# Kernel optimization log

Measured on AMD Instinct MI355X. Metric: run time of the kernel, lower is better.

The kernel has to match this reference:

```python
import jax, jax.numpy as jnp
import numpy as np

N_ENT = 50000
N_REL = 200
DIM = 128
N_BASES = 4
NUM_RELATIONS = 2 * N_REL  # RGCNConv num_relations
E = 200000
S = 20000


def rgcn_conv(x, edge_index, edge_type, edge_norm, basis, att, root, bias, n_nodes):
    """RGCNConv with basis decomposition, aggr='mean'.
    x: [N, Din]; basis: [B, Din, Dout]; att: [R, B]; root: [Din, Dout]; bias: [Dout].
    """
    src, dst = edge_index[0], edge_index[1]
    x_j = x[src]                      # [E, Din] gather
    att_e = att[edge_type]            # [E, B]
    # message: x_j @ (att_e @ basis) without materializing per-edge [Din,Dout] weights
    msg = jnp.einsum('ei,bio,eb->eo', x_j, basis, att_e)  # [E, Dout]
    msg = msg * edge_norm[:, None]
    agg = jax.ops.segment_sum(msg, dst, num_segments=n_nodes)            # [N, Dout]
    cnt = jax.ops.segment_sum(jnp.ones_like(edge_norm), dst, num_segments=n_nodes)
    agg = agg / jnp.maximum(cnt, 1.0)[:, None]            # mean aggregation
    return agg + x @ root + bias


def setup_inputs() -> dict:
    key = jax.random.key(0)
    ks = jax.random.split(key, 20)
    d = {}
    d['entity'] = jnp.arange(N_ENT, dtype=jnp.int64) if jax.config.read('jax_enable_x64') else jnp.arange(N_ENT, dtype=jnp.int32)
    d['edge_index'] = jax.random.randint(ks[0], (2, E), 0, N_ENT)
    d['edge_type'] = jax.random.randint(ks[1], (E,), 0, NUM_RELATIONS)
    d['edge_norm'] = jax.random.uniform(ks[2], (E,), dtype=jnp.float32)
    d['samples'] = jax.random.randint(ks[3], (S, 3), 0, N_REL)
    d['DAD_rel'] = jax.random.normal(ks[4], (N_REL, N_REL), dtype=jnp.float32) * 0.05
    # learned parameters
    d['entity_emb'] = jax.random.normal(ks[5], (N_ENT, DIM), dtype=jnp.float32) * 0.02
    d['relation_emb'] = jax.random.normal(ks[6], (N_REL, DIM), dtype=jnp.float32) * 0.02
    d['entity_context_tab'] = jax.random.normal(ks[7], (N_ENT, DIM), dtype=jnp.float32) * 0.02
    d['relation_context_tab'] = jax.random.normal(ks[8], (N_REL, DIM), dtype=jnp.float32) * 0.02
    d['relation_gcn_weight'] = jax.random.normal(ks[9], (DIM, DIM), dtype=jnp.float32) * 0.02
    d['gate_entity'] = jax.random.uniform(ks[10], (DIM,), dtype=jnp.float32)
    d['gate_relation'] = jax.random.uniform(ks[11], (DIM,), dtype=jnp.float32)
    d['basis1'] = jax.random.normal(ks[12], (N_BASES, DIM, DIM), dtype=jnp.float32) * 0.02
    d['att1'] = jax.random.normal(ks[13], (NUM_RELATIONS, N_BASES), dtype=jnp.float32) * 0.1
    d['root1'] = jax.random.normal(ks[14], (DIM, DIM), dtype=jnp.float32) * 0.02
    d['bias1'] = jnp.zeros((DIM,), dtype=jnp.float32)
    d['basis2'] = jax.random.normal(ks[15], (N_BASES, DIM, DIM), dtype=jnp.float32) * 0.02
    d['att2'] = jax.random.normal(ks[16], (NUM_RELATIONS, N_BASES), dtype=jnp.float32) * 0.1
    d['root2'] = jax.random.normal(ks[17], (DIM, DIM), dtype=jnp.float32) * 0.02
    d['bias2'] = jnp.zeros((DIM,), dtype=jnp.float32)
    return d


def reference(entity, edge_index, edge_type, edge_norm, samples, DAD_rel,
              entity_emb, relation_emb, entity_context_tab, relation_context_tab,
              relation_gcn_weight, gate_entity, gate_relation,
              basis1, att1, root1, bias1, basis2, att2, root2, bias2):
    n_nodes = entity.shape[0]
    ent_ctx = entity_context_tab[entity]                  # [N, D]
    rel_ctx = relation_context_tab                        # arange over all relations -> full table
    ent_ctx = jax.nn.relu(rgcn_conv(ent_ctx, edge_index, edge_type, edge_norm,
                                    basis1, att1, root1, bias1, n_nodes))
    ent_ctx = jax.nn.relu(rgcn_conv(ent_ctx, edge_index, edge_type, edge_norm,
                                    basis2, att2, root2, bias2, n_nodes))
    rel_ctx = jax.nn.relu((DAD_rel @ rel_ctx) @ relation_gcn_weight)
    ge = jax.nn.sigmoid(gate_entity)
    gr = jax.nn.sigmoid(gate_relation)
    h, r, t = samples[:, 0], samples[:, 1], samples[:, 2]
    head_o = ge * entity_emb[h] + (1.0 - ge) * ent_ctx[h]
    rel_o = gr * relation_emb[r] + (1.0 - gr) * rel_ctx[r]
    tail_o = ge * entity_emb[t] + (1.0 - ge) * ent_ctx[t]
    return jnp.stack([head_o, rel_o, tail_o])             # [3, S, D]
```

## Files before the change

kernel.cpp:

```cpp
#include <hip/hip_runtime.h>
#include <hip/hip_bf16.h>

typedef short s8v  __attribute__((ext_vector_type(8)));
typedef float f16v __attribute__((ext_vector_type(16)));

__device__ __forceinline__ unsigned short f2bf(float x) {
    unsigned u = __float_as_uint(x);
    unsigned r = ((u >> 16) & 1u) + 0x7FFFu;
    return (unsigned short)((u + r) >> 16);
}
__device__ __forceinline__ float bf2f(unsigned short h) {
    return __uint_as_float(((unsigned)h) << 16);
}

__global__ __launch_bounds__(256) void x0_kernel(
    const float* __restrict__ tab, const int* __restrict__ entity,
    float* __restrict__ X0, int N)
{
    int idx = blockIdx.x * 256 + threadIdx.x;
    int n = idx >> 5, l = idx & 31;
    if (n < N) {
        int src = entity[n];
        *(float4*)&X0[(size_t)n * 128 + l * 4] =
            *(const float4*)&tab[(size_t)src * 128 + l * 4];
    }
}

__global__ __launch_bounds__(256) void bprep_kernel(
    const float* __restrict__ basis1, const float* __restrict__ root1,
    const float* __restrict__ basis2, const float* __restrict__ root2,
    unsigned short* __restrict__ Bp1h, unsigned short* __restrict__ Bp1l,
    unsigned short* __restrict__ Bp2h, unsigned short* __restrict__ Bp2l)
{
    int idx = blockIdx.x * 256 + threadIdx.x;
    int layer = blockIdx.y;
    int n = idx & 127, k = idx >> 7;
    const float* basis = layer ? basis2 : basis1;
    const float* root  = layer ? root2  : root1;
    float v = (k < 512) ? basis[((k & 3) << 14) + ((k >> 2) << 7) + n]
                        : root[((k - 512) << 7) + n];
    unsigned short h = f2bf(v);
    unsigned short l = f2bf(v - bf2f(h));
    size_t pos = (((size_t)(k >> 3) * 128) + n) * 8 + (k & 7);
    unsigned short* Bh = layer ? Bp2h : Bp1h;
    unsigned short* Bl = layer ? Bp2l : Bp1l;
    Bh[pos] = h;
    Bl[pos] = l;
}

__global__ __launch_bounds__(256) void hist_kernel(
    const int* __restrict__ edge_index, int* __restrict__ deg, int E)
{
    int e = blockIdx.x * 256 + threadIdx.x;
    if (e < E) atomicAdd(&deg[edge_index[E + e]], 1);
}

__global__ __launch_bounds__(1024) void scanA_kernel(
    const int* __restrict__ deg, int* __restrict__ row_start,
    int* __restrict__ btot, int N)
{
    __shared__ int wtot[16];
    __shared__ int woff[16];
    const int tid = threadIdx.x, lane = tid & 63, wid = tid >> 6;
    int i = blockIdx.x * 1024 + tid;
    int v = (i < N) ? deg[i] : 0;
    int x = v;
    #pragma unroll
    for (int d = 1; d < 64; d <<= 1) {
        int t = __shfl_up(x, d, 64);
        if (lane >= d) x += t;
    }
    if (lane == 63) wtot[wid] = x;
    __syncthreads();
    if (wid == 0 && lane < 16) {
        int s = wtot[lane];
        int y = s;
        #pragma unroll
        for (int d = 1; d < 16; d <<= 1) {
            int t = __shfl_up(y, d, 16);
            if (lane >= d) y += t;
        }
        woff[lane] = y - s;
        if (lane == 15) btot[blockIdx.x] = y;
    }
    __syncthreads();
    if (i < N) row_start[i] = woff[wid] + (x - v);
}

__global__ __launch_bounds__(64) void scanB_kernel(
    const int* __restrict__ btot, int* __restrict__ boff,
    int* __restrict__ row_start, int nB, int N)
{
    int t = threadIdx.x;
    int v = (t < nB) ? btot[t] : 0;
    int x = v;
    #pragma unroll
    for (int d = 1; d < 64; d <<= 1) {
        int u = __shfl_up(x, d, 64);
        if (t >= d) x += u;
    }
    if (t < nB) boff[t] = x - v;
    if (t == nB - 1) row_start[N] = x;
}

__global__ __launch_bounds__(1024) void scanC_kernel(
    int* __restrict__ row_start, int* __restrict__ cursor,
    const int* __restrict__ boff, int N)
{
    int i = blockIdx.x * 1024 + threadIdx.x;
    if (i < N) {
        int r = row_start[i] + boff[blockIdx.x];
        row_start[i] = r;
        cursor[i]    = r;
    }
}

__global__ __launch_bounds__(256) void fill_kernel(
    const int* __restrict__ edge_index, const int* __restrict__ edge_type,
    const float* __restrict__ edge_norm, int* __restrict__ cursor,
    const float* __restrict__ att1, const float* __restrict__ att2,
    int* __restrict__ src_s, float4* __restrict__ an1, float4* __restrict__ an2, int E)
{
    int e = blockIdx.x * 256 + threadIdx.x;
    if (e >= E) return;
    int dst = edge_index[E + e];
    int et  = edge_type[e];
    float n = edge_norm[e];
    int pos = atomicAdd(&cursor[dst], 1);
    src_s[pos] = edge_index[e];
    float4 a1 = *(const float4*)&att1[(size_t)et * 4];
    float4 a2 = *(const float4*)&att2[(size_t)et * 4];
    an1[pos] = make_float4(n * a1.x, n * a1.y, n * a1.z, n * a1.w);
    an2[pos] = make_float4(n * a2.x, n * a2.y, n * a2.z, n * a2.w);
}

__global__ __launch_bounds__(256) void edge_agg_kernel(
    const float* __restrict__ X,
    const int* __restrict__ row_start,
    const int* __restrict__ src_s,
    const float4* __restrict__ an,
    unsigned short* __restrict__ w, int N)
{
    int n = blockIdx.x * 8 + (threadIdx.x >> 5);
    if (n >= N) return;
    int l = threadIdx.x & 31;
    int s0 = row_start[n], s1 = row_start[n + 1];
    float acc[4][4];
    #pragma unroll
    for (int d = 0; d < 4; ++d)
        #pragma unroll
        for (int b = 0; b < 4; ++b) acc[d][b] = 0.f;

    for (int p = s0; p < s1; p += 4) {
        int i1 = min(p + 1, s1 - 1);
        int i2 = min(p + 2, s1 - 1);
        int i3 = min(p + 3, s1 - 1);
        int sA = src_s[p],  sB = src_s[i1];
        int sC = src_s[i2], sD = src_s[i3];
        float4 aA = an[p],  aB = an[i1];
        float4 aC = an[i2], aD = an[i3];
        if (p + 1 >= s1) aB = make_float4(0.f, 0.f, 0.f, 0.f);
        if (p + 2 >= s1) aC = make_float4(0.f, 0.f, 0.f, 0.f);
        if (p + 3 >= s1) aD = make_float4(0.f, 0.f, 0.f, 0.f);
        float4 xA = *(const float4*)&X[(size_t)sA * 128 + (l << 2)];
        float4 xB = *(const float4*)&X[(size_t)sB * 128 + (l << 2)];
        float4 xC = *(const float4*)&X[(size_t)sC * 128 + (l << 2)];
        float4 xD = *(const float4*)&X[(size_t)sD * 128 + (l << 2)];
        float xsA[4] = {xA.x, xA.y, xA.z, xA.w};
        float xsB[4] = {xB.x, xB.y, xB.z, xB.w};
        float xsC[4] = {xC.x, xC.y, xC.z, xC.w};
        float xsD[4] = {xD.x, xD.y, xD.z, xD.w};
        #pragma unroll
        for (int d = 0; d < 4; ++d) {
            acc[d][0] = fmaf(aA.x, xsA[d], fmaf(aB.x, xsB[d], fmaf(aC.x, xsC[d], fmaf(aD.x, xsD[d], acc[d][0]))));
            acc[d][1] = fmaf(aA.y, xsA[d], fmaf(aB.y, xsB[d], fmaf(aC.y, xsC[d], fmaf(aD.y, xsD[d], acc[d][1]))));
            acc[d][2] = fmaf(aA.z, xsA[d], fmaf(aB.z, xsB[d], fmaf(aC.z, xsC[d], fmaf(aD.z, xsD[d], acc[d][2]))));
            acc[d][3] = fmaf(aA.w, xsA[d], fmaf(aB.w, xsB[d], fmaf(aC.w, xsC[d], fmaf(aD.w, xsD[d], acc[d][3]))));
        }
    }
    float inv = 1.0f / fmaxf((float)(s1 - s0), 1.0f);
    #pragma unroll
    for (int d = 0; d < 4; ++d) {
        ushort4 h;
        h.x = f2bf(acc[d][0] * inv);
        h.y = f2bf(acc[d][1] * inv);
        h.z = f2bf(acc[d][2] * inv);
        h.w = f2bf(acc[d][3] * inv);
        *(ushort4*)&w[(size_t)n * 512 + (l << 4) + (d << 2)] = h;
    }
}

__global__ __launch_bounds__(256) void gemm640_kernel(
    const unsigned short* __restrict__ wbf,
    const float* __restrict__ X,
    const unsigned short* __restrict__ Bph,
    const unsigned short* __restrict__ Bpl,
    const float* __restrict__ bias,
    float* __restrict__ Xout, int N)
{
    __shared__ unsigned short A_hi[64 * 40];
    __shared__ unsigned short A_lo[64 * 40];

    const int tid  = threadIdx.x;
    const int row0 = blockIdx.x * 64;
    const int lane = tid & 63, wv = tid >> 6;
    const int m    = lane & 31;
    const int kh8  = lane >> 5;
    const int rt   = (wv & 1) << 5;
    const int c0w  = (wv >> 1) << 6;

    const int ar  = tid >> 2;
    const int akv = (tid & 3) << 3;

    const s8v z8 = {0,0,0,0,0,0,0,0};
    s8v pA = z8;
    float4 pX0, pX1;
    s8v B0[8], B1[8];

    auto loadB = [&](int kc, s8v (&dst)[8]) {
        #pragma unroll
        for (int h = 0; h < 2; ++h) {
            int khg = kc * 4 + h * 2 + kh8;
            #pragma unroll
            for (int ct = 0; ct < 2; ++ct) {
                size_t off = ((size_t)khg * 128 + (c0w + ct * 32 + m)) * 8;
                dst[h * 4 + ct * 2 + 0] = *(const s8v*)&Bph[off];
                dst[h * 4 + ct * 2 + 1] = *(const s8v*)&Bpl[off];
            }
        }
    };
    auto loadA = [&](int kc) {
        int k0 = kc * 32;
        int gr = row0 + ar;
        if (k0 < 512) {
            pA = (gr < N) ? *(const s8v*)&wbf[(size_t)gr * 512 + k0 + akv] : z8;
        } else {
            pX0 = make_float4(0.f, 0.f, 0.f, 0.f);
            pX1 = pX0;
            if (gr < N) {
                pX0 = *(const float4*)&X[(size_t)gr * 128 + (k0 - 512) + akv];
                pX1 = *(const float4*)&X[(size_t)gr * 128 + (k0 - 512) + akv + 4];
            }
        }
    };

    f16v acc0, acc1;
    #pragma unroll
    for (int i = 0; i < 16; ++i) { acc0[i] = 0.f; acc1[i] = 0.f; }

    loadA(0);
    loadB(0, B0);

    auto chunk = [&](int kc, s8v (&cur)[8], s8v (&nxt)[8]) {
        const int k0 = kc * 32;
        if (kc) __syncthreads();
        if (k0 < 512) {
            *(s8v*)&A_hi[ar * 40 + akv] = pA;
        } else {
            float f[8] = {pX0.x, pX0.y, pX0.z, pX0.w, pX1.x, pX1.y, pX1.z, pX1.w};
            s8v h8, l8;
            #pragma unroll
            for (int j = 0; j < 8; ++j) {
                unsigned short h = f2bf(f[j]);
                h8[j] = (short)h;
                l8[j] = (short)f2bf(f[j] - bf2f(h));
            }
            *(s8v*)&A_hi[ar * 40 + akv] = h8;
            *(s8v*)&A_lo[ar * 40 + akv] = l8;
        }
        __syncthreads();
        if (kc < 19) { loadA(kc + 1); loadB(kc + 1, nxt); }

        #pragma unroll
        for (int h = 0; h < 2; ++h) {
            const int off = h * 16 + kh8 * 8;
            s8v aH = *(const s8v*)&A_hi[(rt + m) * 40 + off];
            if (k0 < 512) {
                acc0 = __builtin_amdgcn_mfma_f32_32x32x16_bf16(aH, cur[h*4+1], acc0, 0, 0, 0);
                acc0 = __builtin_amdgcn_mfma_f32_32x32x16_bf16(aH, cur[h*4+0], acc0, 0, 0, 0);
                acc1 = __builtin_amdgcn_mfma_f32_32x32x16_bf16(aH, cur[h*4+3], acc1, 0, 0, 0);
                acc1 = __builtin_amdgcn_mfma_f32_32x32x16_bf16(aH, cur[h*4+2], acc1, 0, 0, 0);
            } else {
                s8v aL = *(const s8v*)&A_lo[(rt + m) * 40 + off];
                acc0 = __builtin_amdgcn_mfma_f32_32x32x16_bf16(aL, cur[h*4+0], acc0, 0, 0, 0);
                acc0 = __builtin_amdgcn_mfma_f32_32x32x16_bf16(aH, cur[h*4+1], acc0, 0, 0, 0);
                acc0 = __builtin_amdgcn_mfma_f32_32x32x16_bf16(aH, cur[h*4+0], acc0, 0, 0, 0);
                acc1 = __builtin_amdgcn_mfma_f32_32x32x16_bf16(aL, cur[h*4+2], acc1, 0, 0, 0);
                acc1 = __builtin_amdgcn_mfma_f32_32x32x16_bf16(aH, cur[h*4+3], acc1, 0, 0, 0);
                acc1 = __builtin_amdgcn_mfma_f32_32x32x16_bf16(aH, cur[h*4+2], acc1, 0, 0, 0);
            }
        }
    };

    #pragma unroll 1
    for (int kc2 = 0; kc2 < 10; ++kc2) {
        chunk(kc2 * 2,     B0, B1);
        chunk(kc2 * 2 + 1, B1, B0);
    }

    const int rbase = rt + (kh8 << 2);
    #pragma unroll
    for (int ct = 0; ct < 2; ++ct) {
        int gc = c0w + ct * 32 + m;
        float bv = bias[gc];
        #pragma unroll
        for (int reg = 0; reg < 16; ++reg) {
            int gr = row0 + rbase + (reg & 3) + ((reg >> 2) << 3);
            if (gr < N) {
                float v = ct ? acc1[reg] : acc0[reg];
                Xout[(size_t)gr * 128 + gc] = fmaxf(v + bv, 0.f);
            }
        }
    }
}

__global__ __launch_bounds__(512) void relctx_kernel(
    const float* __restrict__ DAD,
    const float* __restrict__ tab,
    const float* __restrict__ W,
    float* __restrict__ R2, int NR)
{
    __shared__ float part[4][128];
    __shared__ float r1s[128];
    int r = blockIdx.x;
    int t = threadIdx.x;
    int o = t & 127, q = t >> 7;
    float s = 0.f;
    #pragma unroll 4
    for (int j = q; j < NR; j += 4)
        s = fmaf(DAD[r * NR + j], tab[j * 128 + o], s);
    part[q][o] = s;
    __syncthreads();
    if (t < 128) r1s[t] = part[0][t] + part[1][t] + part[2][t] + part[3][t];
    __syncthreads();
    float s2 = 0.f;
    #pragma unroll 8
    for (int k = q * 32; k < q * 32 + 32; ++k)
        s2 = fmaf(r1s[k], W[k * 128 + o], s2);
    part[q][o] = s2;
    __syncthreads();
    if (t < 128)
        R2[r * 128 + t] = fmaxf(part[0][t] + part[1][t] + part[2][t] + part[3][t], 0.f);
}

__global__ __launch_bounds__(256) void output_kernel(
    const int* __restrict__ samples,
    const float* __restrict__ gate_e,
    const float* __restrict__ gate_r,
    const float* __restrict__ ent_emb,
    const float* __restrict__ rel_emb,
    const float* __restrict__ ctx2,
    const float* __restrict__ relctx,
    float* __restrict__ out, int S)
{
    int s = blockIdx.x * 2 + (threadIdx.x >> 7);
    if (s >= S) return;
    int p = blockIdx.y;
    int o = threadIdx.x & 127;
    float v;
    if (p == 1) {
        int idx = samples[s * 3 + 1];
        float g = 1.0f / (1.0f + __expf(-gate_r[o]));
        v = g * rel_emb[idx * 128 + o] + (1.0f - g) * relctx[idx * 128 + o];
    } else {
        int idx = samples[s * 3 + (p == 0 ? 0 : 2)];
        float g = 1.0f / (1.0f + __expf(-gate_e[o]));
        v = g * ent_emb[(size_t)idx * 128 + o] + (1.0f - g) * ctx2[(size_t)idx * 128 + o];
    }
    out[(size_t)p * S * 128 + (size_t)s * 128 + o] = v;
}

extern "C" void kernel_launch(void* const* d_in, const int* in_sizes, int n_in,
                              void* d_out, int out_size, void* d_ws, size_t ws_size,
                              hipStream_t stream)
{
    const int*   entity     = (const int*)d_in[0];
    const int*   edge_index = (const int*)d_in[1];
    const int*   edge_type  = (const int*)d_in[2];
    const float* edge_norm  = (const float*)d_in[3];
    const int*   samples    = (const int*)d_in[4];
    const float* DAD        = (const float*)d_in[5];
    const float* ent_emb    = (const float*)d_in[6];
    const float* rel_emb    = (const float*)d_in[7];
    const float* ent_tab    = (const float*)d_in[8];
    const float* rel_tab    = (const float*)d_in[9];
    const float* Wrel       = (const float*)d_in[10];
    const float* gate_e     = (const float*)d_in[11];
    const float* gate_r     = (const float*)d_in[12];
    const float* basis1     = (const float*)d_in[13];
    const float* att1       = (const float*)d_in[14];
    const float* root1      = (const float*)d_in[15];
    const float* bias1      = (const float*)d_in[16];
    const float* basis2     = (const float*)d_in[17];
    const float* att2       = (const float*)d_in[18];
    const float* root2      = (const float*)d_in[19];
    const float* bias2      = (const float*)d_in[20];

    const int N  = in_sizes[0];
    const int E  = in_sizes[2];
    const int S  = in_sizes[4] / 3;
    const int NR = in_sizes[9] / 128;

    float* ws      = (float*)d_ws;
    float* X0      = ws;
    float* X1      = X0 + (size_t)N * 128;
    float4* an1    = (float4*)(X1 + (size_t)N * 128);
    float4* an2    = an1 + (E + 4);
    unsigned short* wbf = (unsigned short*)(an2 + (E + 4));
    float* Rc      = (float*)(wbf + (size_t)N * 512);
    int*   deg     = (int*)(Rc + (size_t)NR * 128);
    int*   rstart  = deg + N;
    int*   cursor  = rstart + N + 1;
    int*   src_s   = cursor + N;
    int*   btot    = src_s + E + 4;
    int*   boff    = btot + 64;
    uintptr_t bt   = ((uintptr_t)(boff + 64) + 15) & ~(uintptr_t)15;
    unsigned short* Bp1h = (unsigned short*)bt;
    unsigned short* Bp1l = Bp1h + 80 * 128 * 8;
    unsigned short* Bp2h = Bp1l + 80 * 128 * 8;
    unsigned short* Bp2l = Bp2h + 80 * 128 * 8;

    const int egrid = (E + 255) / 256;
    const int ggrid = (N + 63) / 64;
    const int agrid = (N + 7) / 8;
    const int nB    = (N + 1023) / 1024;

    bprep_kernel<<<dim3(320, 2), 256, 0, stream>>>(basis1, root1, basis2, root2,
                                                   Bp1h, Bp1l, Bp2h, Bp2l);
    hipMemsetAsync(deg, 0, (size_t)N * sizeof(int), stream);
    hist_kernel<<<egrid, 256, 0, stream>>>(edge_index, deg, E);
    scanA_kernel<<<nB, 1024, 0, stream>>>(deg, rstart, btot, N);
    scanB_kernel<<<1, 64, 0, stream>>>(btot, boff, rstart, nB, N);
    scanC_kernel<<<nB, 1024, 0, stream>>>(rstart, cursor, boff, N);
    fill_kernel<<<egrid, 256, 0, stream>>>(edge_index, edge_type, edge_norm, cursor,
                                           att1, att2, src_s, an1, an2, E);

    x0_kernel<<<(N * 32 + 255) / 256, 256, 0, stream>>>(ent_tab, entity, X0, N);

    edge_agg_kernel<<<agrid, 256, 0, stream>>>(X0, rstart, src_s, an1, wbf, N);
    gemm640_kernel<<<ggrid, 256, 0, stream>>>(wbf, X0, Bp1h, Bp1l, bias1, X1, N);

    edge_agg_kernel<<<agrid, 256, 0, stream>>>(X1, rstart, src_s, an2, wbf, N);
    gemm640_kernel<<<ggrid, 256, 0, stream>>>(wbf, X1, Bp2h, Bp2l, bias2, X0, N);

    relctx_kernel<<<NR, 512, 0, stream>>>(DAD, rel_tab, Wrel, Rc, NR);

    output_kernel<<<dim3((S + 1) / 2, 3), 256, 0, stream>>>(
        samples, gate_e, gate_r, ent_emb, rel_emb, X0, Rc, (float*)d_out, S);
}
```

Measured before the change: 348.2 us.

## Fuse edge aggregation and basis GEMM into one per-layer kernel via LDS

Merges the edge gather/aggregation kernel and the 640-wide MFMA GEMM into a single layer kernel. Each block aggregates 32 nodes into a swizzled LDS tile holding the bf16 basis coefficients plus the hi/lo split of the root input, then runs the MFMA GEMM directly from LDS. This removes the global round-trip of the N x 512 bf16 intermediate and one launch per layer. In exchange, the GEMM tile shrinks from 64 to 32 rows with 32 columns per wave, so the B matrix is reloaded for every 32 rows. The block also needs about 48KB of LDS, which may lower occupancy during the latency-bound gather phase.

```diff
diff --git a/kernel.cpp b/kernel.cpp
--- a/kernel.cpp
+++ b/kernel.cpp
@@ -134,183 +134,158 @@
     an2[pos] = make_float4(n * a2.x, n * a2.y, n * a2.z, n * a2.w);
 }
 
-__global__ __launch_bounds__(256) void edge_agg_kernel(
+__global__ __launch_bounds__(256) void layer_kernel(
     const float* __restrict__ X,
     const int* __restrict__ row_start,
     const int* __restrict__ src_s,
     const float4* __restrict__ an,
-    unsigned short* __restrict__ w, int N)
-{
-    int n = blockIdx.x * 8 + (threadIdx.x >> 5);
-    if (n >= N) return;
-    int l = threadIdx.x & 31;
-    int s0 = row_start[n], s1 = row_start[n + 1];
-    float acc[4][4];
-    #pragma unroll
-    for (int d = 0; d < 4; ++d)
-        #pragma unroll
-        for (int b = 0; b < 4; ++b) acc[d][b] = 0.f;
-
-    for (int p = s0; p < s1; p += 4) {
-        int i1 = min(p + 1, s1 - 1);
-        int i2 = min(p + 2, s1 - 1);
-        int i3 = min(p + 3, s1 - 1);
-        int sA = src_s[p],  sB = src_s[i1];
-        int sC = src_s[i2], sD = src_s[i3];
-        float4 aA = an[p],  aB = an[i1];
-        float4 aC = an[i2], aD = an[i3];
-        if (p + 1 >= s1) aB = make_float4(0.f, 0.f, 0.f, 0.f);
-        if (p + 2 >= s1) aC = make_float4(0.f, 0.f, 0.f, 0.f);
-        if (p + 3 >= s1) aD = make_float4(0.f, 0.f, 0.f, 0.f);
-        float4 xA = *(const float4*)&X[(size_t)sA * 128 + (l << 2)];
-        float4 xB = *(const float4*)&X[(size_t)sB * 128 + (l << 2)];
-        float4 xC = *(const float4*)&X[(size_t)sC * 128 + (l << 2)];
-        float4 xD = *(const float4*)&X[(size_t)sD * 128 + (l << 2)];
-        float xsA[4] = {xA.x, xA.y, xA.z, xA.w};
-        float xsB[4] = {xB.x, xB.y, xB.z, xB.w};
-        float xsC[4] = {xC.x, xC.y, xC.z, xC.w};
-        float xsD[4] = {xD.x, xD.y, xD.z, xD.w};
-        #pragma unroll
-        for (int d = 0; d < 4; ++d) {
-            acc[d][0] = fmaf(aA.x, xsA[d], fmaf(aB.x, xsB[d], fmaf(aC.x, xsC[d], fmaf(aD.x, xsD[d], acc[d][0]))));
-            acc[d][1] = fmaf(aA.y, xsA[d], fmaf(aB.y, xsB[d], fmaf(aC.y, xsC[d], fmaf(aD.y, xsD[d], acc[d][1]))));
-            acc[d][2] = fmaf(aA.z, xsA[d], fmaf(aB.z, xsB[d], fmaf(aC.z, xsC[d], fmaf(aD.z, xsD[d], acc[d][2]))));
-            acc[d][3] = fmaf(aA.w, xsA[d], fmaf(aB.w, xsB[d], fmaf(aC.w, xsC[d], fmaf(aD.w, xsD[d], acc[d][3]))));
-        }
-    }
-    float inv = 1.0f / fmaxf((float)(s1 - s0), 1.0f);
-    #pragma unroll
-    for (int d = 0; d < 4; ++d) {
-        ushort4 h;
-        h.x = f2bf(acc[d][0] * inv);
-        h.y = f2bf(acc[d][1] * inv);
-        h.z = f2bf(acc[d][2] * inv);
-        h.w = f2bf(acc[d][3] * inv);
-        *(ushort4*)&w[(size_t)n * 512 + (l << 4) + (d << 2)] = h;
-    }
-}
-
-__global__ __launch_bounds__(256) void gemm640_kernel(
-    const unsigned short* __restrict__ wbf,
-    const float* __restrict__ X,
     const unsigned short* __restrict__ Bph,
     const unsigned short* __restrict__ Bpl,
     const float* __restrict__ bias,
     float* __restrict__ Xout, int N)
 {
-    __shared__ unsigned short A_hi[64 * 40];
-    __shared__ unsigned short A_lo[64 * 40];
-
-    const int tid  = threadIdx.x;
-    const int row0 = blockIdx.x * 64;
+    __shared__ unsigned short Whi[80 * 32 * 8];
+    __shared__ unsigned short Wlo[16 * 32 * 8];
+
+    const int tid   = threadIdx.x;
+    const int node0 = blockIdx.x * 32;
+
+    {
+        int g = tid >> 5, l = tid & 31;
+        #pragma unroll 1
+        for (int i = 0; i < 4; ++i) {
+            int n  = g * 4 + i;
+            int gn = node0 + n;
+            float acc[4][4];
+            #pragma unroll
+            for (int d = 0; d < 4; ++d)
+                #pragma unroll
+                for (int b = 0; b < 4; ++b) acc[d][b] = 0.f;
+            float inv = 1.f;
+            if (gn < N) {
+                int s0 = row_start[gn], s1 = row_start[gn + 1];
+                for (int p = s0; p < s1; p += 4) {
+                    int i1 = min(p + 1, s1 - 1);
+                    int i2 = min(p + 2, s1 - 1);
+                    int i3 = min(p + 3, s1 - 1);
+                    int sA = src_s[p],  sB = src_s[i1];
+                    int sC = src_s[i2], sD = src_s[i3];
+                    float4 aA = an[p],  aB = an[i1];
+                    float4 aC = an[i2], aD = an[i3];
+                    if (p + 1 >= s1) aB = make_float4(0.f, 0.f, 0.f, 0.f);
+                    if (p + 2 >= s1) aC = make_float4(0.f, 0.f, 0.f, 0.f);
+                    if (p + 3 >= s1) aD = make_float4(0.f, 0.f, 0.f, 0.f);
+                    float4 xA = *(const float4*)&X[(size_t)sA * 128 + (l << 2)];
+                    float4 xB = *(const float4*)&X[(size_t)sB * 128 + (l << 2)];
+                    float4 xC = *(const float4*)&X[(size_t)sC * 128 + (l << 2)];
+                    float4 xD = *(const float4*)&X[(size_t)sD * 128 + (l << 2)];
+                    float xsA[4] = {xA.x, xA.y, xA.z, xA.w};
+                    float xsB[4] = {xB.x, xB.y, xB.z, xB.w};
+                    float xsC[4] = {xC.x, xC.y, xC.z, xC.w};
+                    float xsD[4] = {xD.x, xD.y, xD.z, xD.w};
+                    #pragma unroll
+                    for (int d = 0; d < 4; ++d) {
+                        acc[d][0] = fmaf(aA.x, xsA[d], fmaf(aB.x, xsB[d], fmaf(aC.x, xsC[d], fmaf(aD.x, xsD[d], acc[d][0]))));
+                        acc[d][1] = fmaf(aA.y, xsA[d], fmaf(aB.y, xsB[d], fmaf(aC.y, xsC[d], fmaf(aD.y, xsD[d], acc[d][1]))));
+                        acc[d][2] = fmaf(aA.z, xsA[d], fmaf(aB.z, xsB[d], fmaf(aC.z, xsC[d], fmaf(aD.z, xsD[d], acc[d][2]))));
+                        acc[d][3] = fmaf(aA.w, xsA[d], fmaf(aB.w, xsB[d], fmaf(aC.w, xsC[d], fmaf(aD.w, xsD[d], acc[d][3]))));
+                    }
+                }
+                inv = 1.0f / fmaxf((float)(s1 - s0), 1.0f);
+            }
+            #pragma unroll
+            for (int d = 0; d < 4; ++d) {
+                int kh   = 2 * l + (d >> 1);
+                int slot = n ^ (kh & 31);
+                ushort4 h;
+                h.x = f2bf(acc[d][0] * inv);
+                h.y = f2bf(acc[d][1] * inv);
+                h.z = f2bf(acc[d][2] * inv);
+                h.w = f2bf(acc[d][3] * inv);
+                *(ushort4*)&Whi[(kh * 32 + slot) * 8 + (d & 1) * 4] = h;
+            }
+        }
+    }
+
+    {
+        int r  = tid >> 3;
+        int kq = (tid & 7) * 16;
+        int gn = node0 + r;
+        float4 v0 = make_float4(0,0,0,0), v1 = v0, v2 = v0, v3 = v0;
+        if (gn < N) {
+            const float* xp = &X[(size_t)gn * 128 + kq];
+            v0 = *(const float4*)(xp + 0);
+            v1 = *(const float4*)(xp + 4);
+            v2 = *(const float4*)(xp + 8);
+            v3 = *(const float4*)(xp + 12);
+        }
+        float f[16] = {v0.x, v0.y, v0.z, v0.w, v1.x, v1.y, v1.z, v1.w,
+                       v2.x, v2.y, v2.z, v2.w, v3.x, v3.y, v3.z, v3.w};
+        #pragma unroll
+        for (int i = 0; i < 2; ++i) {
+            int kh   = 64 + (tid & 7) * 2 + i;
+            int slot = r ^ (kh & 31);
+            s8v h8, l8;
+            #pragma unroll
+            for (int j = 0; j < 8; ++j) {
+                unsigned short h = f2bf(f[i * 8 + j]);
+                h8[j] = (short)h;
+                l8[j] = (short)f2bf(f[i * 8 + j] - bf2f(h));
+            }
+            *(s8v*)&Whi[(kh * 32 + slot) * 8] = h8;
+            *(s8v*)&Wlo[((kh - 64) * 32 + slot) * 8] = l8;
+        }
+    }
+    __syncthreads();
+
     const int lane = tid & 63, wv = tid >> 6;
     const int m    = lane & 31;
     const int kh8  = lane >> 5;
-    const int rt   = (wv & 1) << 5;
-    const int c0w  = (wv >> 1) << 6;
-
-    const int ar  = tid >> 2;
-    const int akv = (tid & 3) << 3;
-
-    const s8v z8 = {0,0,0,0,0,0,0,0};
-    s8v pA = z8;
-    float4 pX0, pX1;
-    s8v B0[8], B1[8];
-
-    auto loadB = [&](int kc, s8v (&dst)[8]) {
+    const int c0   = wv << 5;
+
+    f16v acc;
+    #pragma unroll
+    for (int i = 0; i < 16; ++i) acc[i] = 0.f;
+
+    s8v Bb[2][8];
+    auto loadB4 = [&](int g, int buf) {
         #pragma unroll
-        for (int h = 0; h < 2; ++h) {
-            int khg = kc * 4 + h * 2 + kh8;
-            #pragma unroll
-            for (int ct = 0; ct < 2; ++ct) {
-                size_t off = ((size_t)khg * 128 + (c0w + ct * 32 + m)) * 8;
-                dst[h * 4 + ct * 2 + 0] = *(const s8v*)&Bph[off];
-                dst[h * 4 + ct * 2 + 1] = *(const s8v*)&Bpl[off];
+        for (int q = 0; q < 4; ++q) {
+            int khg = (g * 4 + q) * 2 + kh8;
+            size_t off = ((size_t)khg * 128 + c0 + m) * 8;
+            Bb[buf][q * 2 + 0] = *(const s8v*)&Bph[off];
+            Bb[buf][q * 2 + 1] = *(const s8v*)&Bpl[off];
+        }
+    };
+    loadB4(0, 0);
+
+    #pragma unroll
+    for (int g = 0; g < 10; ++g) {
+        int buf = g & 1;
+        if (g < 9) loadB4(g + 1, buf ^ 1);
+        #pragma unroll
+        for (int q = 0; q < 4; ++q) {
+            int s    = g * 4 + q;
+            int khg  = s * 2 + kh8;
+            int slot = m ^ (khg & 31);
+            s8v aH = *(const s8v*)&Whi[(khg * 32 + slot) * 8];
+            if (s >= 32) {
+                s8v aL = *(const s8v*)&Wlo[((khg - 64) * 32 + slot) * 8];
+                acc = __builtin_amdgcn_mfma_f32_32x32x16_bf16(aL, Bb[buf][q*2], acc, 0, 0, 0);
             }
-        }
-    };
-    auto loadA = [&](int kc) {
-        int k0 = kc * 32;
-        int gr = row0 + ar;
-        if (k0 < 512) {
-            pA = (gr < N) ? *(const s8v*)&wbf[(size_t)gr * 512 + k0 + akv] : z8;
-        } else {
-            pX0 = make_float4(0.f, 0.f, 0.f, 0.f);
-            pX1 = pX0;
-            if (gr < N) {
-                pX0 = *(const float4*)&X[(size_t)gr * 128 + (k0 - 512) + akv];
-                pX1 = *(const float4*)&X[(size_t)gr * 128 + (k0 - 512) + akv + 4];
-            }
-        }
-    };
-
-    f16v acc0, acc1;
+            acc = __builtin_amdgcn_mfma_f32_32x32x16_bf16(aH, Bb[buf][q*2+1], acc, 0, 0, 0);
+            acc = __builtin_amdgcn_mfma_f32_32x32x16_bf16(aH, Bb[buf][q*2+0], acc, 0, 0, 0);
+        }
+    }
+
+    int gc = c0 + m;
+    float bv = bias[gc];
+    const int rbase = kh8 << 2;
     #pragma unroll
-    for (int i = 0; i < 16; ++i) { acc0[i] = 0.f; acc1[i] = 0.f; }
-
-    loadA(0);
-    loadB(0, B0);
-
-    auto chunk = [&](int kc, s8v (&cur)[8], s8v (&nxt)[8]) {
-        const int k0 = kc * 32;
-        if (kc) __syncthreads();
-        if (k0 < 512) {
-            *(s8v*)&A_hi[ar * 40 + akv] = pA;
-        } else {
-            float f[8] = {pX0.x, pX0.y, pX0.z, pX0.w, pX1.x, pX1.y, pX1.z, pX1.w};
-            s8v h8, l8;
-            #pragma unroll
-            for (int j = 0; j < 8; ++j) {
-                unsigned short h = f2bf(f[j]);
-                h8[j] = (short)h;
-                l8[j] = (short)f2bf(f[j] - bf2f(h));
-            }
-            *(s8v*)&A_hi[ar * 40 + akv] = h8;
-            *(s8v*)&A_lo[ar * 40 + akv] = l8;
-        }
-        __syncthreads();
-        if (kc < 19) { loadA(kc + 1); loadB(kc + 1, nxt); }
-
-        #pragma unroll
-        for (int h = 0; h < 2; ++h) {
-            const int off = h * 16 + kh8 * 8;
-            s8v aH = *(const s8v*)&A_hi[(rt + m) * 40 + off];
-            if (k0 < 512) {
-                acc0 = __builtin_amdgcn_mfma_f32_32x32x16_bf16(aH, cur[h*4+1], acc0, 0, 0, 0);
-                acc0 = __builtin_amdgcn_mfma_f32_32x32x16_bf16(aH, cur[h*4+0], acc0, 0, 0, 0);
-                acc1 = __builtin_amdgcn_mfma_f32_32x32x16_bf16(aH, cur[h*4+3], acc1, 0, 0, 0);
-                acc1 = __builtin_amdgcn_mfma_f32_32x32x16_bf16(aH, cur[h*4+2], acc1, 0, 0, 0);
-            } else {
-                s8v aL = *(const s8v*)&A_lo[(rt + m) * 40 + off];
-                acc0 = __builtin_amdgcn_mfma_f32_32x32x16_bf16(aL, cur[h*4+0], acc0, 0, 0, 0);
-                acc0 = __builtin_amdgcn_mfma_f32_32x32x16_bf16(aH, cur[h*4+1], acc0, 0, 0, 0);
-                acc0 = __builtin_amdgcn_mfma_f32_32x32x16_bf16(aH, cur[h*4+0], acc0, 0, 0, 0);
-                acc1 = __builtin_amdgcn_mfma_f32_32x32x16_bf16(aL, cur[h*4+2], acc1, 0, 0, 0);
-                acc1 = __builtin_amdgcn_mfma_f32_32x32x16_bf16(aH, cur[h*4+3], acc1, 0, 0, 0);
-                acc1 = __builtin_amdgcn_mfma_f32_32x32x16_bf16(aH, cur[h*4+2], acc1, 0, 0, 0);
-            }
-        }
-    };
-
-    #pragma unroll 1
-    for (int kc2 = 0; kc2 < 10; ++kc2) {
-        chunk(kc2 * 2,     B0, B1);
-        chunk(kc2 * 2 + 1, B1, B0);
-    }
-
-    const int rbase = rt + (kh8 << 2);
-    #pragma unroll
-    for (int ct = 0; ct < 2; ++ct) {
-        int gc = c0w + ct * 32 + m;
-        float bv = bias[gc];
-        #pragma unroll
-        for (int reg = 0; reg < 16; ++reg) {
-            int gr = row0 + rbase + (reg & 3) + ((reg >> 2) << 3);
-            if (gr < N) {
-                float v = ct ? acc1[reg] : acc0[reg];
-                Xout[(size_t)gr * 128 + gc] = fmaxf(v + bv, 0.f);
-            }
-        }
+    for (int reg = 0; reg < 16; ++reg) {
+        int gr = node0 + rbase + (reg & 3) + ((reg >> 2) << 3);
+        if (gr < N)
+            Xout[(size_t)gr * 128 + gc] = fmaxf(acc[reg] + bv, 0.f);
     }
 }
 
@@ -406,8 +381,7 @@
     float* X1      = X0 + (size_t)N * 128;
     float4* an1    = (float4*)(X1 + (size_t)N * 128);
     float4* an2    = an1 + (E + 4);
-    unsigned short* wbf = (unsigned short*)(an2 + (E + 4));
-    float* Rc      = (float*)(wbf + (size_t)N * 512);
+    float* Rc      = (float*)(an2 + (E + 4));
     int*   deg     = (int*)(Rc + (size_t)NR * 128);
     int*   rstart  = deg + N;
     int*   cursor  = rstart + N + 1;
@@ -421,8 +395,7 @@
     unsigned short* Bp2l = Bp2h + 80 * 128 * 8;
 
     const int egrid = (E + 255) / 256;
-    const int ggrid = (N + 63) / 64;
-    const int agrid = (N + 7) / 8;
+    const int lgrid = (N + 31) / 32;
     const int nB    = (N + 1023) / 1024;
 
     bprep_kernel<<<dim3(320, 2), 256, 0, stream>>>(basis1, root1, basis2, root2,
@@ -437,11 +410,9 @@
 
     x0_kernel<<<(N * 32 + 255) / 256, 256, 0, stream>>>(ent_tab, entity, X0, N);
 
-    edge_agg_kernel<<<agrid, 256, 0, stream>>>(X0, rstart, src_s, an1, wbf, N);
-    gemm640_kernel<<<ggrid, 256, 0, stream>>>(wbf, X0, Bp1h, Bp1l, bias1, X1, N);
-
-    edge_agg_kernel<<<agrid, 256, 0, stream>>>(X1, rstart, src_s, an2, wbf, N);
-    gemm640_kernel<<<ggrid, 256, 0, stream>>>(wbf, X1, Bp2h, Bp2l, bias2, X0, N);
+    layer_kernel<<<lgrid, 256, 0, stream>>>(X0, rstart, src_s, an1, Bp1h, Bp1l, bias1, X1, N);
+
+    layer_kernel<<<lgrid, 256, 0, stream>>>(X1, rstart, src_s, an2, Bp2h, Bp2l, bias2, X0, N);
 
     relctx_kernel<<<NR, 512, 0, stream>>>(DAD, rel_tab, Wrel, Rc, NR);
 
```

New measurement: 302.0 us. 13.3% less time.
